# Optimization experiments

Measured on AMD Instinct MI355X. Metric: run time of the kernel, lower is better.

## Reference

```python
import jax, jax.numpy as jnp
import numpy as np

DIM = 2048
N_HEADS = 16
N_KV_HEADS = 4
HEAD_DIM = 128
BASE = 1000.0
B, S = 2, 2048


def setup_inputs() -> dict:
    key = jax.random.key(0)
    ks = jax.random.split(key, 5)
    x = jax.random.normal(ks[0], (B, S, DIM), jnp.float32)
    scale = 1.0 / np.sqrt(DIM)
    Wq = jax.random.normal(ks[1], (DIM, N_HEADS * HEAD_DIM), jnp.float32) * scale
    Wk = jax.random.normal(ks[2], (DIM, N_KV_HEADS * HEAD_DIM), jnp.float32) * scale
    Wv = jax.random.normal(ks[3], (DIM, N_KV_HEADS * HEAD_DIM), jnp.float32) * scale
    Wo = jax.random.normal(ks[4], (N_HEADS * HEAD_DIM, DIM), jnp.float32) * scale
    mask = jnp.tril(jnp.ones((S, S), jnp.int32))  # causal mask from module-level constant
    return {"x": x, "Wq": Wq, "Wk": Wk, "Wv": Wv, "Wo": Wo, "mask": mask}


def _rope_tables(seq_len, head_dim, dtype):
    theta = 1.0 / BASE ** (jnp.arange(0, head_dim, 2, dtype=dtype) / head_dim)
    freqs = jnp.outer(jnp.arange(seq_len, dtype=dtype), theta)  # [S, D/2]
    # broadcast to [1, S, 1, D/2] over (batch, seq, heads, pairs)
    return jnp.cos(freqs)[None, :, None, :], jnp.sin(freqs)[None, :, None, :]


def _apply_rope(x, cos, sin):
    # interleaved RoPE: pairs (x[...,2i], x[...,2i+1])
    x1, x2 = x[..., ::2], x[..., 1::2]
    out = jnp.stack([x1 * cos - x2 * sin, x1 * sin + x2 * cos], axis=-1)
    return out.reshape(x.shape)


def reference(x, Wq, Wk, Wv, Wo, mask):
    batch, seq_len, _ = x.shape
    g = N_HEADS // N_KV_HEADS  # GQA repeat factor
    q = (x @ Wq).reshape(batch, seq_len, N_HEADS, HEAD_DIM)
    k = (x @ Wk).reshape(batch, seq_len, N_KV_HEADS, HEAD_DIM)
    v = (x @ Wv).reshape(batch, seq_len, N_KV_HEADS, HEAD_DIM)
    cos, sin = _rope_tables(seq_len, HEAD_DIM, x.dtype)
    q = _apply_rope(q, cos, sin)
    k = _apply_rope(k, cos, sin)
    # grouped-query attention without materializing repeated K/V:
    # q -> [b, s, kv, g, d]; scores -> [b, kv, g, q, kseq]
    q = q.reshape(batch, seq_len, N_KV_HEADS, g, HEAD_DIM)
    scale = HEAD_DIM ** -0.5
    scores = jnp.einsum("bqhgd,bkhd->bhgqk", q, k) * scale
    scores = jnp.where(mask == 0, float("-inf"), scores)
    attn = jax.nn.softmax(scores, axis=-1)
    out = jnp.einsum("bhgqk,bkhd->bqhgd", attn, v)
    out = out.reshape(batch, seq_len, N_HEADS * HEAD_DIM)
    return out @ Wo
```

## Files before the change

kernel.cpp:

```cpp
#include <hip/hip_runtime.h>
#include <hip/hip_bf16.h>

#define B_    2
#define S_    2048
#define DIM_  2048
#define H_    16
#define HKV_  4
#define D_    128
#define NQKV_ 3072
#define BS_   (B_*S_)

typedef __attribute__((ext_vector_type(8))) short short8;
typedef __attribute__((ext_vector_type(4))) float f32x4;

__device__ __forceinline__ unsigned short f2bf(float f) {
    union { float f; unsigned u; } v; v.f = f;
    unsigned r = (v.u + 0x7fffu + ((v.u >> 16) & 1u)) >> 16;
    return (unsigned short)r;
}
__device__ __forceinline__ float bf2f(unsigned short h) {
    union { unsigned u; float f; } v; v.u = ((unsigned)h) << 16;
    return v.f;
}

__global__ void k_convert(const float* __restrict__ in, unsigned short* __restrict__ out, int n4) {
    int i = blockIdx.x * blockDim.x + threadIdx.x;
    if (i >= n4) return;
    float4 v = ((const float4*)in)[i];
    union { unsigned short us[4]; unsigned long long u; } o;
    o.us[0] = f2bf(v.x); o.us[1] = f2bf(v.y); o.us[2] = f2bf(v.z); o.us[3] = f2bf(v.w);
    ((unsigned long long*)out)[i] = o.u;
}

__global__ void k_transpose(const float* __restrict__ W, unsigned short* __restrict__ WT,
                            int K, int N) {
    __shared__ float tile[64][65];
    const int k0 = blockIdx.x * 64, n0 = blockIdx.y * 64;
    const int tx = threadIdx.x & 63, ty = threadIdx.x >> 6;
    #pragma unroll
    for (int i = 0; i < 64; i += 4)
        tile[ty + i][tx] = W[(size_t)(k0 + ty + i) * N + n0 + tx];
    __syncthreads();
    #pragma unroll
    for (int i = 0; i < 64; i += 4)
        WT[(size_t)(n0 + ty + i) * K + k0 + tx] = f2bf(tile[tx][ty + i]);
}

template<typename OUT_T>
__global__ __launch_bounds__(256, 2)
void k_gemm_bt(const unsigned short* __restrict__ A,
               const unsigned short* __restrict__ BT,
               OUT_T* __restrict__ C, int M, int N, int K)
{
    __shared__ unsigned short lds_a[128 * 32];
    __shared__ unsigned short lds_b[128 * 32];
    const int tid  = threadIdx.x;
    const int nbn  = N >> 7;
    const int nwg  = gridDim.x;
    const int orig = blockIdx.x;
    const int q8   = nwg >> 3, r8 = nwg & 7;
    const int xcd  = orig & 7, lid = orig >> 3;
    const int wgid = (xcd < r8 ? xcd * (q8 + 1) : r8 * (q8 + 1) + (xcd - r8) * q8) + lid;
    const int bm   = wgid / nbn, bn = wgid % nbn;
    const int row0 = bm << 7, col0 = bn << 7;
    const int lane = tid & 63, wave = tid >> 6;
    const int wr = wave >> 1, wc = wave & 1;
    const int lg = lane >> 4, lr = lane & 15;

    f32x4 acc[4][4] = {};

    for (int kt = 0; kt < K; kt += 32) {
        __syncthreads();
        #pragma unroll
        for (int issue = 0; issue < 2; ++issue) {
            int e = issue * 2048 + wave * 512 + lane * 8;
            int r = e >> 5, kk = e & 31;
            const unsigned short* srcA = A  + (size_t)(row0 + r) * K + kt + kk;
            const unsigned short* srcB = BT + (size_t)(col0 + r) * K + kt + kk;
            unsigned short* dstA = lds_a + issue * 2048 + wave * 512;
            unsigned short* dstB = lds_b + issue * 2048 + wave * 512;
            __builtin_amdgcn_global_load_lds(
                (const __attribute__((address_space(1))) void*)srcA,
                (__attribute__((address_space(3))) void*)dstA, 16, 0, 0);
            __builtin_amdgcn_global_load_lds(
                (const __attribute__((address_space(1))) void*)srcB,
                (__attribute__((address_space(3))) void*)dstB, 16, 0, 0);
        }
        __syncthreads();
        short8 af[4], bf[4];
        #pragma unroll
        for (int m = 0; m < 4; ++m)
            af[m] = *(const short8*)&lds_a[(wr * 64 + m * 16 + lr) * 32 + lg * 8];
        #pragma unroll
        for (int n = 0; n < 4; ++n)
            bf[n] = *(const short8*)&lds_b[(wc * 64 + n * 16 + lr) * 32 + lg * 8];
        #pragma unroll
        for (int m = 0; m < 4; ++m)
            #pragma unroll
            for (int n = 0; n < 4; ++n)
                acc[m][n] = __builtin_amdgcn_mfma_f32_16x16x32_bf16(af[m], bf[n], acc[m][n], 0, 0, 0);
    }

    #pragma unroll
    for (int m = 0; m < 4; ++m)
        #pragma unroll
        for (int n = 0; n < 4; ++n)
            #pragma unroll
            for (int j = 0; j < 4; ++j) {
                int row = row0 + wr * 64 + m * 16 + lg * 4 + j;
                int col = col0 + wc * 64 + n * 16 + lr;
                if constexpr (sizeof(OUT_T) == 2)
                    C[(size_t)row * N + col] = (OUT_T)f2bf(acc[m][n][j]);
                else
                    C[(size_t)row * N + col] = (OUT_T)acc[m][n][j];
            }
}

__global__ void k_rope(unsigned short* __restrict__ qkv) {
    const int pair = blockIdx.x * 256 + threadIdx.x;
    const int row  = blockIdx.y;
    const int s    = row & (S_ - 1);
    const int col  = pair * 2;
    const int t    = (col & 127) >> 1;
    const float theta = exp2f(-((float)(2 * t) / 128.0f) * 9.965784284662087f);
    const float ang = (float)s * theta;
    const float sn = sinf(ang), cs = cosf(ang);
    unsigned short* p = qkv + (size_t)row * NQKV_ + col;
    float x1 = bf2f(p[0]), x2 = bf2f(p[1]);
    p[0] = f2bf(x1 * cs - x2 * sn);
    p[1] = f2bf(x1 * sn + x2 * cs);
}

__global__ void k_vtrans(const unsigned short* __restrict__ qkv, unsigned short* __restrict__ vt) {
    __shared__ unsigned short tile[64][65];
    const int s0 = blockIdx.x * 64;
    const int d0 = blockIdx.y * 64;
    const int bh = blockIdx.z;
    const int b = bh >> 2, hk = bh & 3;
    const int tx = threadIdx.x & 63, ty = threadIdx.x >> 6;
    #pragma unroll
    for (int i = 0; i < 64; i += 4)
        tile[i + ty][tx] = qkv[(size_t)(b * S_ + s0 + i + ty) * NQKV_ + (DIM_ + 512) + hk * D_ + d0 + tx];
    __syncthreads();
    #pragma unroll
    for (int i = 0; i < 64; i += 4)
        vt[((size_t)bh * D_ + d0 + i + ty) * S_ + s0 + tx] = tile[tx][i + ty];
}

#define KPAD 136
#define VPAD 72
__global__ __launch_bounds__(512, 4)
void k_attn(const unsigned short* __restrict__ qkv,
            const unsigned short* __restrict__ vt,
            unsigned short* __restrict__ o)
{
    __shared__ unsigned short k_lds[64 * KPAD];
    __shared__ unsigned short v_lds[128 * VPAD];
    __shared__ unsigned short p_lds[8 * 16 * VPAD];

    const int qt = blockIdx.x, h = blockIdx.y, b = blockIdx.z;
    const int tid = threadIdx.x;
    const int lane = tid & 63, wave = tid >> 6;
    const int lg = lane >> 4, lr = lane & 15;
    const int hk = h >> 2;
    const int qb = qt * 128;
    const int q_base = qb + wave * 16;
    const int nt = qt * 2 + 2;
    const int my_nt = ((q_base + 15) >> 6) + 1;

    short8 qf[4];
    {
        const unsigned short* qrow = qkv + (size_t)(b * S_ + q_base + lr) * NQKV_ + h * D_;
        #pragma unroll
        for (int dc = 0; dc < 4; ++dc)
            qf[dc] = *(const short8*)(qrow + dc * 32 + lg * 8);
    }

    float m_run[4], l_run[4];
    #pragma unroll
    for (int j = 0; j < 4; ++j) { m_run[j] = -1e30f; l_run[j] = 0.f; }
    f32x4 oacc[8] = {};

    const unsigned short* kglob = qkv + (size_t)(b * S_) * NQKV_ + DIM_ + hk * D_;
    const unsigned short* vglob = vt + (size_t)(b * HKV_ + hk) * D_ * S_;
    unsigned short* p_my = p_lds + wave * 16 * VPAD;
    const float scale = 0.08838834764831845f;

    for (int kt = 0; kt < nt; ++kt) {
        const int k0 = kt * 64;
        const int id1 = tid + 512;
        short8 ks0 = *(const short8*)(kglob + (size_t)(k0 + (tid >> 4)) * NQKV_ + (tid & 15) * 8);
        short8 ks1 = *(const short8*)(kglob + (size_t)(k0 + (id1 >> 4)) * NQKV_ + (id1 & 15) * 8);
        short8 vs0 = *(const short8*)(vglob + (size_t)(tid >> 3) * S_ + k0 + (tid & 7) * 8);
        short8 vs1 = *(const short8*)(vglob + (size_t)(id1 >> 3) * S_ + k0 + (id1 & 7) * 8);
        __syncthreads();
        *(short8*)&k_lds[(tid >> 4) * KPAD + (tid & 15) * 8] = ks0;
        *(short8*)&k_lds[(id1 >> 4) * KPAD + (id1 & 15) * 8] = ks1;
        *(short8*)&v_lds[(tid >> 3) * VPAD + (tid & 7) * 8] = vs0;
        *(short8*)&v_lds[(id1 >> 3) * VPAD + (id1 & 7) * 8] = vs1;
        __syncthreads();

        if (kt >= my_nt) continue;

        f32x4 sc[4];
        #pragma unroll
        for (int f = 0; f < 4; ++f) sc[f] = (f32x4){0.f, 0.f, 0.f, 0.f};
        #pragma unroll
        for (int f = 0; f < 4; ++f)
            #pragma unroll
            for (int dc = 0; dc < 4; ++dc) {
                short8 kf = *(const short8*)&k_lds[(f * 16 + lr) * KPAD + dc * 32 + lg * 8];
                sc[f] = __builtin_amdgcn_mfma_f32_16x16x32_bf16(qf[dc], kf, sc[f], 0, 0, 0);
            }
        #pragma unroll
        for (int f = 0; f < 4; ++f) {
            int kpos = k0 + f * 16 + lr;
            #pragma unroll
            for (int j = 0; j < 4; ++j) {
                int qpos = q_base + lg * 4 + j;
                float s = sc[f][j] * scale;
                sc[f][j] = (kpos <= qpos) ? s : -1e30f;
            }
        }
        #pragma unroll
        for (int j = 0; j < 4; ++j) {
            float mx = fmaxf(fmaxf(sc[0][j], sc[1][j]), fmaxf(sc[2][j], sc[3][j]));
            #pragma unroll
            for (int off = 1; off < 16; off <<= 1) mx = fmaxf(mx, __shfl_xor(mx, off));
            float mnew = fmaxf(m_run[j], mx);
            float corr = __expf(m_run[j] - mnew);
            float p0 = __expf(sc[0][j] - mnew);
            float p1 = __expf(sc[1][j] - mnew);
            float p2 = __expf(sc[2][j] - mnew);
            float p3 = __expf(sc[3][j] - mnew);
            float rs = (p0 + p1) + (p2 + p3);
            #pragma unroll
            for (int off = 1; off < 16; off <<= 1) rs += __shfl_xor(rs, off);
            l_run[j] = l_run[j] * corr + rs;
            m_run[j] = mnew;
            #pragma unroll
            for (int c = 0; c < 8; ++c) oacc[c][j] *= corr;
            int prow = (lg * 4 + j) * VPAD;
            p_my[prow + lr]      = f2bf(p0);
            p_my[prow + 16 + lr] = f2bf(p1);
            p_my[prow + 32 + lr] = f2bf(p2);
            p_my[prow + 48 + lr] = f2bf(p3);
        }
        asm volatile("s_waitcnt lgkmcnt(0)" ::: "memory");
        #pragma unroll
        for (int kh = 0; kh < 2; ++kh) {
            short8 pf = *(const short8*)&p_my[lr * VPAD + kh * 32 + lg * 8];
            #pragma unroll
            for (int c = 0; c < 8; ++c) {
                short8 vf = *(const short8*)&v_lds[(c * 16 + lr) * VPAD + kh * 32 + lg * 8];
                oacc[c] = __builtin_amdgcn_mfma_f32_16x16x32_bf16(pf, vf, oacc[c], 0, 0, 0);
            }
        }
    }

    #pragma unroll
    for (int j = 0; j < 4; ++j) {
        float inv = 1.0f / l_run[j];
        #pragma unroll
        for (int c = 0; c < 8; ++c)
            o[(size_t)(b * S_ + q_base + lg * 4 + j) * DIM_ + h * D_ + c * 16 + lr] =
                f2bf(oacc[c][j] * inv);
    }
}

extern "C" void kernel_launch(void* const* d_in, const int* in_sizes, int n_in,
                              void* d_out, int out_size, void* d_ws, size_t ws_size,
                              hipStream_t stream)
{
    const float* x  = (const float*)d_in[0];
    const float* Wq = (const float*)d_in[1];
    const float* Wk = (const float*)d_in[2];
    const float* Wv = (const float*)d_in[3];
    const float* Wo = (const float*)d_in[4];
    float* out = (float*)d_out;

    char* ws = (char*)d_ws;
    unsigned short* xb    = (unsigned short*)(ws);
    unsigned short* wqkvt = (unsigned short*)(ws + 16777216);
    unsigned short* wot   = (unsigned short*)(ws + 29360128);
    unsigned short* qkv   = (unsigned short*)(ws + 37748736);
    unsigned short* vt    = (unsigned short*)(ws + 62914560);
    unsigned short* attno = (unsigned short*)(ws + 67108864);

    k_convert<<<(BS_ * DIM_ / 4) / 256, 256, 0, stream>>>(x, xb, BS_ * DIM_ / 4);

    k_transpose<<<dim3(DIM_ / 64, DIM_ / 64), 256, 0, stream>>>(Wq, wqkvt, DIM_, 2048);
    k_transpose<<<dim3(DIM_ / 64, 512 / 64), 256, 0, stream>>>(Wk, wqkvt + (size_t)2048 * 2048, DIM_, 512);
    k_transpose<<<dim3(DIM_ / 64, 512 / 64), 256, 0, stream>>>(Wv, wqkvt + (size_t)2560 * 2048, DIM_, 512);
    k_transpose<<<dim3(DIM_ / 64, DIM_ / 64), 256, 0, stream>>>(Wo, wot, 2048, 2048);

    k_gemm_bt<unsigned short><<<(BS_ / 128) * (NQKV_ / 128), 256, 0, stream>>>(
        xb, wqkvt, qkv, BS_, NQKV_, DIM_);

    k_rope<<<dim3(5, BS_), 256, 0, stream>>>(qkv);

    k_vtrans<<<dim3(S_ / 64, D_ / 64, B_ * HKV_), 256, 0, stream>>>(qkv, vt);

    k_attn<<<dim3(S_ / 128, H_, B_), 512, 0, stream>>>(qkv, vt, attno);

    k_gemm_bt<float><<<(BS_ / 128) * (DIM_ / 128), 256, 0, stream>>>(
        attno, wot, out, BS_, DIM_, DIM_);
}
```

Before: 406.0 us.

## Restructure attention with transposed scores, register prefetch, and deeper GEMM k-tile

The attention kernel now uses 64-query tiles with 256 threads and a flattened grid that pairs heavy and light causal tiles. It computes transposed scores (K×Q) so each lane owns one query row, which allows the softmax in exp2 with a prescaled log2e factor and replaces the LDS round-trip for P with register shuffles. K/V loads for the next tile are issued into registers before the current tile is computed, and only the diagonal tile is masked. Separately, the GEMM k-step is doubled to 64 to halve barrier count, at the cost of more LDS per block.

New measurement: 383.2 us. 5.6% less time.

```diff
diff --git a/kernel.cpp b/kernel.cpp
--- a/kernel.cpp
+++ b/kernel.cpp
@@ -52,8 +52,8 @@
                const unsigned short* __restrict__ BT,
                OUT_T* __restrict__ C, int M, int N, int K)
 {
-    __shared__ unsigned short lds_a[128 * 32];
-    __shared__ unsigned short lds_b[128 * 32];
+    __shared__ unsigned short lds_a[128 * 64];
+    __shared__ unsigned short lds_b[128 * 64];
     const int tid  = threadIdx.x;
     const int nbn  = N >> 7;
     const int nwg  = gridDim.x;
@@ -69,12 +69,12 @@
 
     f32x4 acc[4][4] = {};
 
-    for (int kt = 0; kt < K; kt += 32) {
+    for (int kt = 0; kt < K; kt += 64) {
         __syncthreads();
         #pragma unroll
-        for (int issue = 0; issue < 2; ++issue) {
+        for (int issue = 0; issue < 4; ++issue) {
             int e = issue * 2048 + wave * 512 + lane * 8;
-            int r = e >> 5, kk = e & 31;
+            int r = e >> 6, kk = e & 63;
             const unsigned short* srcA = A  + (size_t)(row0 + r) * K + kt + kk;
             const unsigned short* srcB = BT + (size_t)(col0 + r) * K + kt + kk;
             unsigned short* dstA = lds_a + issue * 2048 + wave * 512;
@@ -87,18 +87,21 @@
                 (__attribute__((address_space(3))) void*)dstB, 16, 0, 0);
         }
         __syncthreads();
-        short8 af[4], bf[4];
-        #pragma unroll
-        for (int m = 0; m < 4; ++m)
-            af[m] = *(const short8*)&lds_a[(wr * 64 + m * 16 + lr) * 32 + lg * 8];
-        #pragma unroll
-        for (int n = 0; n < 4; ++n)
-            bf[n] = *(const short8*)&lds_b[(wc * 64 + n * 16 + lr) * 32 + lg * 8];
-        #pragma unroll
-        for (int m = 0; m < 4; ++m)
+        #pragma unroll
+        for (int kc = 0; kc < 2; ++kc) {
+            short8 af[4], bf[4];
+            #pragma unroll
+            for (int m = 0; m < 4; ++m)
+                af[m] = *(const short8*)&lds_a[(wr * 64 + m * 16 + lr) * 64 + kc * 32 + lg * 8];
             #pragma unroll
             for (int n = 0; n < 4; ++n)
-                acc[m][n] = __builtin_amdgcn_mfma_f32_16x16x32_bf16(af[m], bf[n], acc[m][n], 0, 0, 0);
+                bf[n] = *(const short8*)&lds_b[(wc * 64 + n * 16 + lr) * 64 + kc * 32 + lg * 8];
+            #pragma unroll
+            for (int m = 0; m < 4; ++m)
+                #pragma unroll
+                for (int n = 0; n < 4; ++n)
+                    acc[m][n] = __builtin_amdgcn_mfma_f32_16x16x32_bf16(af[m], bf[n], acc[m][n], 0, 0, 0);
+        }
     }
 
     #pragma unroll
@@ -149,24 +152,40 @@
 
 #define KPAD 136
 #define VPAD 72
-__global__ __launch_bounds__(512, 4)
+#define SCALE2 0.12751739f
+
+#define STAGE_LOAD(K0) do {                                                                    \
+    ks0 = *(const short8*)(kglob + (size_t)((K0) + (tid >> 4)) * NQKV_ + (tid & 15) * 8);      \
+    ks1 = *(const short8*)(kglob + (size_t)((K0) + 16 + (tid >> 4)) * NQKV_ + (tid & 15) * 8); \
+    ks2 = *(const short8*)(kglob + (size_t)((K0) + 32 + (tid >> 4)) * NQKV_ + (tid & 15) * 8); \
+    ks3 = *(const short8*)(kglob + (size_t)((K0) + 48 + (tid >> 4)) * NQKV_ + (tid & 15) * 8); \
+    vs0 = *(const short8*)(vglob + (size_t)(tid >> 3) * S_ + (K0) + (tid & 7) * 8);            \
+    vs1 = *(const short8*)(vglob + (size_t)(32 + (tid >> 3)) * S_ + (K0) + (tid & 7) * 8);     \
+    vs2 = *(const short8*)(vglob + (size_t)(64 + (tid >> 3)) * S_ + (K0) + (tid & 7) * 8);     \
+    vs3 = *(const short8*)(vglob + (size_t)(96 + (tid >> 3)) * S_ + (K0) + (tid & 7) * 8);     \
+} while (0)
+
+__global__ __launch_bounds__(256, 4)
 void k_attn(const unsigned short* __restrict__ qkv,
             const unsigned short* __restrict__ vt,
             unsigned short* __restrict__ o)
 {
     __shared__ unsigned short k_lds[64 * KPAD];
     __shared__ unsigned short v_lds[128 * VPAD];
-    __shared__ unsigned short p_lds[8 * 16 * VPAD];
-
-    const int qt = blockIdx.x, h = blockIdx.y, b = blockIdx.z;
+
+    const int L   = blockIdx.x;
+    const int w4  = L >> 8;
+    const int c   = L & 255;
+    const int qt0 = c & 31;
+    const int hb  = (c >> 5) | (w4 << 3);
+    const int h   = hb & 15, b = hb >> 4;
+    const int qt  = (w4 & 1) ? (31 - qt0) : qt0;
+    const int hk  = h >> 2;
+
     const int tid = threadIdx.x;
     const int lane = tid & 63, wave = tid >> 6;
     const int lg = lane >> 4, lr = lane & 15;
-    const int hk = h >> 2;
-    const int qb = qt * 128;
-    const int q_base = qb + wave * 16;
-    const int nt = qt * 2 + 2;
-    const int my_nt = ((q_base + 15) >> 6) + 1;
+    const int q_base = qt * 64 + wave * 16;
 
     short8 qf[4];
     {
@@ -176,31 +195,28 @@
             qf[dc] = *(const short8*)(qrow + dc * 32 + lg * 8);
     }
 
-    float m_run[4], l_run[4];
-    #pragma unroll
-    for (int j = 0; j < 4; ++j) { m_run[j] = -1e30f; l_run[j] = 0.f; }
+    float m_run = -1e30f, l_run = 0.f;
     f32x4 oacc[8] = {};
 
     const unsigned short* kglob = qkv + (size_t)(b * S_) * NQKV_ + DIM_ + hk * D_;
     const unsigned short* vglob = vt + (size_t)(b * HKV_ + hk) * D_ * S_;
-    unsigned short* p_my = p_lds + wave * 16 * VPAD;
-    const float scale = 0.08838834764831845f;
-
-    for (int kt = 0; kt < nt; ++kt) {
-        const int k0 = kt * 64;
-        const int id1 = tid + 512;
-        short8 ks0 = *(const short8*)(kglob + (size_t)(k0 + (tid >> 4)) * NQKV_ + (tid & 15) * 8);
-        short8 ks1 = *(const short8*)(kglob + (size_t)(k0 + (id1 >> 4)) * NQKV_ + (id1 & 15) * 8);
-        short8 vs0 = *(const short8*)(vglob + (size_t)(tid >> 3) * S_ + k0 + (tid & 7) * 8);
-        short8 vs1 = *(const short8*)(vglob + (size_t)(id1 >> 3) * S_ + k0 + (id1 & 7) * 8);
+
+    short8 ks0, ks1, ks2, ks3, vs0, vs1, vs2, vs3;
+    STAGE_LOAD(0);
+
+    for (int t = 0; t <= qt; ++t) {
+        const int k0 = t * 64;
         __syncthreads();
-        *(short8*)&k_lds[(tid >> 4) * KPAD + (tid & 15) * 8] = ks0;
-        *(short8*)&k_lds[(id1 >> 4) * KPAD + (id1 & 15) * 8] = ks1;
-        *(short8*)&v_lds[(tid >> 3) * VPAD + (tid & 7) * 8] = vs0;
-        *(short8*)&v_lds[(id1 >> 3) * VPAD + (id1 & 7) * 8] = vs1;
+        *(short8*)&k_lds[((tid >> 4)     ) * KPAD + (tid & 15) * 8] = ks0;
+        *(short8*)&k_lds[((tid >> 4) + 16) * KPAD + (tid & 15) * 8] = ks1;
+        *(short8*)&k_lds[((tid >> 4) + 32) * KPAD + (tid & 15) * 8] = ks2;
+        *(short8*)&k_lds[((tid >> 4) + 48) * KPAD + (tid & 15) * 8] = ks3;
+        *(short8*)&v_lds[((tid >> 3)     ) * VPAD + (tid & 7) * 8] = vs0;
+        *(short8*)&v_lds[((tid >> 3) + 32) * VPAD + (tid & 7) * 8] = vs1;
+        *(short8*)&v_lds[((tid >> 3) + 64) * VPAD + (tid & 7) * 8] = vs2;
+        *(short8*)&v_lds[((tid >> 3) + 96) * VPAD + (tid & 7) * 8] = vs3;
         __syncthreads();
-
-        if (kt >= my_nt) continue;
+        if (t < qt) { STAGE_LOAD(k0 + 64); }
 
         f32x4 sc[4];
         #pragma unroll
@@ -210,61 +226,85 @@
             #pragma unroll
             for (int dc = 0; dc < 4; ++dc) {
                 short8 kf = *(const short8*)&k_lds[(f * 16 + lr) * KPAD + dc * 32 + lg * 8];
-                sc[f] = __builtin_amdgcn_mfma_f32_16x16x32_bf16(qf[dc], kf, sc[f], 0, 0, 0);
+                sc[f] = __builtin_amdgcn_mfma_f32_16x16x32_bf16(kf, qf[dc], sc[f], 0, 0, 0);
             }
+        float mxl = -1e30f;
+        if (t == qt) {
+            const int qpos = q_base + lr;
+            #pragma unroll
+            for (int f = 0; f < 4; ++f)
+                #pragma unroll
+                for (int j = 0; j < 4; ++j) {
+                    int kpos = k0 + f * 16 + lg * 4 + j;
+                    float s = sc[f][j] * SCALE2;
+                    sc[f][j] = (kpos <= qpos) ? s : -1e30f;
+                    mxl = fmaxf(mxl, sc[f][j]);
+                }
+        } else {
+            #pragma unroll
+            for (int f = 0; f < 4; ++f)
+                #pragma unroll
+                for (int j = 0; j < 4; ++j) {
+                    sc[f][j] *= SCALE2;
+                    mxl = fmaxf(mxl, sc[f][j]);
+                }
+        }
+        mxl = fmaxf(mxl, __shfl_xor(mxl, 16));
+        mxl = fmaxf(mxl, __shfl_xor(mxl, 32));
+        float mnew = fmaxf(m_run, mxl);
+        float corr = exp2f(m_run - mnew);
+        m_run = mnew;
+        float rs = 0.f;
+        #pragma unroll
+        for (int f = 0; f < 4; ++f)
+            #pragma unroll
+            for (int j = 0; j < 4; ++j) {
+                sc[f][j] = exp2f(sc[f][j] - mnew);
+                rs += sc[f][j];
+            }
+        rs += __shfl_xor(rs, 16);
+        rs += __shfl_xor(rs, 32);
+        l_run = l_run * corr + rs;
+        #pragma unroll
+        for (int cc = 0; cc < 8; ++cc)
+            #pragma unroll
+            for (int j = 0; j < 4; ++j) oacc[cc][j] *= corr;
+        unsigned pk[4][2];
         #pragma unroll
         for (int f = 0; f < 4; ++f) {
-            int kpos = k0 + f * 16 + lr;
-            #pragma unroll
-            for (int j = 0; j < 4; ++j) {
-                int qpos = q_base + lg * 4 + j;
-                float s = sc[f][j] * scale;
-                sc[f][j] = (kpos <= qpos) ? s : -1e30f;
+            pk[f][0] = (unsigned)f2bf(sc[f][0]) | ((unsigned)f2bf(sc[f][1]) << 16);
+            pk[f][1] = (unsigned)f2bf(sc[f][2]) | ((unsigned)f2bf(sc[f][3]) << 16);
+        }
+        const int srcA = (lg & 1) * 32 + lr;
+        const int srcB = srcA + 16;
+        const bool hiF = ((lg >> 1) != 0);
+        #pragma unroll
+        for (int kh = 0; kh < 2; ++kh) {
+            unsigned a0 = __shfl(pk[2 * kh][0], srcA), b0 = __shfl(pk[2 * kh + 1][0], srcA);
+            unsigned a1 = __shfl(pk[2 * kh][1], srcA), b1 = __shfl(pk[2 * kh + 1][1], srcA);
+            unsigned a2 = __shfl(pk[2 * kh][0], srcB), b2 = __shfl(pk[2 * kh + 1][0], srcB);
+            unsigned a3 = __shfl(pk[2 * kh][1], srcB), b3 = __shfl(pk[2 * kh + 1][1], srcB);
+            union { unsigned u[4]; short8 s8; } pf_;
+            pf_.u[0] = hiF ? b0 : a0; pf_.u[1] = hiF ? b1 : a1;
+            pf_.u[2] = hiF ? b2 : a2; pf_.u[3] = hiF ? b3 : a3;
+            #pragma unroll
+            for (int cc = 0; cc < 8; ++cc) {
+                short8 vf = *(const short8*)&v_lds[(cc * 16 + lr) * VPAD + kh * 32 + lg * 8];
+                oacc[cc] = __builtin_amdgcn_mfma_f32_16x16x32_bf16(vf, pf_.s8, oacc[cc], 0, 0, 0);
             }
         }
-        #pragma unroll
-        for (int j = 0; j < 4; ++j) {
-            float mx = fmaxf(fmaxf(sc[0][j], sc[1][j]), fmaxf(sc[2][j], sc[3][j]));
-            #pragma unroll
-            for (int off = 1; off < 16; off <<= 1) mx = fmaxf(mx, __shfl_xor(mx, off));
-            float mnew = fmaxf(m_run[j], mx);
-            float corr = __expf(m_run[j] - mnew);
-            float p0 = __expf(sc[0][j] - mnew);
-            float p1 = __expf(sc[1][j] - mnew);
-            float p2 = __expf(sc[2][j] - mnew);
-            float p3 = __expf(sc[3][j] - mnew);
-            float rs = (p0 + p1) + (p2 + p3);
-            #pragma unroll
-            for (int off = 1; off < 16; off <<= 1) rs += __shfl_xor(rs, off);
-            l_run[j] = l_run[j] * corr + rs;
-            m_run[j] = mnew;
-            #pragma unroll
-            for (int c = 0; c < 8; ++c) oacc[c][j] *= corr;
-            int prow = (lg * 4 + j) * VPAD;
-            p_my[prow + lr]      = f2bf(p0);
-            p_my[prow + 16 + lr] = f2bf(p1);
-            p_my[prow + 32 + lr] = f2bf(p2);
-            p_my[prow + 48 + lr] = f2bf(p3);
-        }
-        asm volatile("s_waitcnt lgkmcnt(0)" ::: "memory");
-        #pragma unroll
-        for (int kh = 0; kh < 2; ++kh) {
-            short8 pf = *(const short8*)&p_my[lr * VPAD + kh * 32 + lg * 8];
-            #pragma unroll
-            for (int c = 0; c < 8; ++c) {
-                short8 vf = *(const short8*)&v_lds[(c * 16 + lr) * VPAD + kh * 32 + lg * 8];
-                oacc[c] = __builtin_amdgcn_mfma_f32_16x16x32_bf16(pf, vf, oacc[c], 0, 0, 0);
-            }
-        }
     }
 
-    #pragma unroll
-    for (int j = 0; j < 4; ++j) {
-        float inv = 1.0f / l_run[j];
-        #pragma unroll
-        for (int c = 0; c < 8; ++c)
-            o[(size_t)(b * S_ + q_base + lg * 4 + j) * DIM_ + h * D_ + c * 16 + lr] =
-                f2bf(oacc[c][j] * inv);
+    {
+        float inv = 1.0f / l_run;
+        unsigned short* orow = o + (size_t)(b * S_ + q_base + lr) * DIM_ + h * D_ + lg * 4;
+        #pragma unroll
+        for (int cc = 0; cc < 8; ++cc) {
+            union { unsigned short us[4]; unsigned long long u; } ov;
+            #pragma unroll
+            for (int j = 0; j < 4; ++j) ov.us[j] = f2bf(oacc[cc][j] * inv);
+            *(unsigned long long*)(orow + cc * 16) = ov.u;
+        }
     }
 }
 
@@ -301,7 +341,7 @@
 
     k_vtrans<<<dim3(S_ / 64, D_ / 64, B_ * HKV_), 256, 0, stream>>>(qkv, vt);
 
-    k_attn<<<dim3(S_ / 128, H_, B_), 512, 0, stream>>>(qkv, vt, attno);
+    k_attn<<<dim3(1024), 256, 0, stream>>>(qkv, vt, attno);
 
     k_gemm_bt<float><<<(BS_ / 128) * (DIM_ / 128), 256, 0, stream>>>(
         attno, wot, out, BS_, DIM_, DIM_);
```
